# Performance work log

Hardware: AMD Instinct MI355X
Metric: run time of the kernel (lower is better)

## Reference

```python
import jax, jax.numpy as jnp
import numpy as np

H = 512  # hidden_dim


def setup_inputs() -> dict:
    key = jax.random.key(0)
    ks = jax.random.split(key, 16)
    inp = {
        "state": jax.random.normal(ks[0], (64,), jnp.float32),
        "p_action": jax.random.normal(ks[1], (4,), jnp.float32),
        "p_reward": jax.random.normal(ks[2], (1,), jnp.float32),
        "timestep": jax.random.normal(ks[3], (1,), jnp.float32),
        "cue": jax.random.normal(ks[4], (H,), jnp.float32),
        "mem_keys": jax.random.normal(ks[5], (100000, H), jnp.float32),
        "mem_vals": jax.random.normal(ks[6], (100000, H), jnp.float32),
        "Wx": jax.random.normal(ks[7], (5 * H, 70), jnp.float32) * 0.05,
        "Wh": jax.random.normal(ks[8], (5 * H, H), jnp.float32) * 0.05,
        "b": jax.random.normal(ks[9], (5 * H,), jnp.float32) * 0.05,
        "actor_w": jax.random.normal(ks[10], (4, H), jnp.float32) * 0.01,
        "actor_b": jnp.zeros((4,), jnp.float32),
        "critic_w": jax.random.normal(ks[11], (1, H), jnp.float32),
        "critic_b": jnp.zeros((1,), jnp.float32),
        "h0": jax.random.normal(ks[12], (H,), jnp.float32),
        "c0": jax.random.normal(ks[13], (H,), jnp.float32),
    }
    return inp


def reference(state, p_action, p_reward, timestep, cue, mem_keys, mem_vals,
              Wx, Wh, b, actor_w, actor_b, critic_w, critic_b, h0, c0):
    # ---- DND.get_memory: l2-kernel softmax-weighted read over memory bank ----
    # sims[n] = -||K[n] - cue||^2 ; m_t = softmax(sims) @ V
    sims = -jnp.sum((mem_keys - cue[None, :]) ** 2, axis=1)  # [N]
    w = jax.nn.softmax(sims)                                  # [N]
    m_t = w @ mem_vals                                        # [H]

    # ---- EpLSTMCell (DND-LSTM cell: gates f,i,o,r + candidate) ----
    x_t = jnp.concatenate([state, p_action, p_reward, timestep])  # [70]
    preact = Wx @ x_t + Wh @ h0 + b                               # [5H]
    gates = jax.nn.sigmoid(preact[: 4 * H])
    f_t, i_t, o_t, r_t = jnp.split(gates, 4)
    c_hat = jnp.tanh(preact[4 * H:])
    c_t = f_t * c0 + i_t * c_hat + r_t * m_t
    h_t = o_t * jnp.tanh(c_t)

    # ---- actor / critic heads ----
    action_dist = jax.nn.softmax(actor_w @ h_t + actor_b)
    value_estimate = critic_w @ h_t + critic_b
    return (action_dist, value_estimate, h_t, c_t)
```

## Files before the change

kernel.cpp:

```cpp
#include <hip/hip_runtime.h>
#include <math.h>

#define HDIM 512
#define NROWS 100000
#define NBLK_A 2048
#define NBLK_B 64

constexpr int SIMS_OFF   = 0;
constexpr int BMIN_OFF   = NROWS;
constexpr int CNT_OFF    = BMIN_OFF + NBLK_A;
constexpr int PREACT_OFF = CNT_OFF + 1;
constexpr int PM_OFF     = PREACT_OFF + 5 * HDIM;
constexpr int PD_OFF     = PM_OFF + NBLK_B * HDIM;

__device__ __forceinline__ float wave_sum(float v) {
    #pragma unroll
    for (int off = 32; off; off >>= 1) v += __shfl_xor(v, off);
    return v;
}
__device__ __forceinline__ float wave_min(float v) {
    #pragma unroll
    for (int off = 32; off; off >>= 1) v = fminf(v, __shfl_xor(v, off));
    return v;
}
__device__ __forceinline__ float d2sum(float4 a, float4 c) {
    float d, s;
    d = a.x - c.x; s  = d * d;
    d = a.y - c.y; s += d * d;
    d = a.z - c.z; s += d * d;
    d = a.w - c.w; s += d * d;
    return s;
}

__global__ __launch_bounds__(256)
void kA(const float* __restrict__ state, const float* __restrict__ pa,
        const float* __restrict__ pr, const float* __restrict__ ts,
        const float* __restrict__ cue, const float* __restrict__ K,
        const float* __restrict__ Wx, const float* __restrict__ Wh,
        const float* __restrict__ b, const float* __restrict__ h0,
        float* __restrict__ ws) {
    if (blockIdx.x == 0 && threadIdx.x == 0)
        ((int*)ws)[CNT_OFF] = 0;

    const int lane = threadIdx.x & 63;
    const int wib  = threadIdx.x >> 6;
    const int gw   = blockIdx.x * 4 + wib;
    const int nw   = NBLK_A * 4;

    if (gw < 5 * HDIM) {
        const int row = gw;
        float x0 = state[lane];
        float x1 = 0.f;
        if      (lane < 4)  x1 = pa[lane];
        else if (lane == 4) x1 = pr[0];
        else if (lane == 5) x1 = ts[0];

        const float4* h04 = (const float4*)h0;
        const float4  hA = h04[lane], hB = h04[64 + lane];
        const float4* wh4 = (const float4*)(Wh + (size_t)row * HDIM);
        const float4 a0 = wh4[lane], a1 = wh4[64 + lane];
        float acc = a0.x*hA.x + a0.y*hA.y + a0.z*hA.z + a0.w*hA.w
                  + a1.x*hB.x + a1.y*hB.y + a1.z*hB.z + a1.w*hB.w;
        const float* wxr = Wx + (size_t)row * 70;
        acc += wxr[lane] * x0;
        if (lane < 6) acc += wxr[64 + lane] * x1;
        acc = wave_sum(acc);
        if (lane == 0) ws[PREACT_OFF + row] = acc + b[row];
    }

    const float4* c4 = (const float4*)cue;
    const float4 cA = c4[lane], cB = c4[64 + lane];
    float minss = INFINITY;

    const int NG = NROWS / 4;
    for (int g = gw; g < NG; g += nw) {
        const int n = g * 4;
        const float* r = K + (size_t)n * HDIM;
        const float4* p0 = (const float4*)(r);
        const float4* p1 = (const float4*)(r + HDIM);
        const float4* p2 = (const float4*)(r + 2 * HDIM);
        const float4* p3 = (const float4*)(r + 3 * HDIM);
        const float4 a0 = p0[lane], b0 = p0[64 + lane];
        const float4 a1 = p1[lane], b1 = p1[64 + lane];
        const float4 a2 = p2[lane], b2 = p2[64 + lane];
        const float4 a3 = p3[lane], b3 = p3[64 + lane];
        float s0 = d2sum(a0, cA) + d2sum(b0, cB);
        float s1 = d2sum(a1, cA) + d2sum(b1, cB);
        float s2 = d2sum(a2, cA) + d2sum(b2, cB);
        float s3 = d2sum(a3, cA) + d2sum(b3, cB);
        #pragma unroll
        for (int off = 32; off; off >>= 1) {
            s0 += __shfl_xor(s0, off);
            s1 += __shfl_xor(s1, off);
            s2 += __shfl_xor(s2, off);
            s3 += __shfl_xor(s3, off);
        }
        if (lane == 0) {
            *(float4*)&ws[SIMS_OFF + n] = make_float4(-s0, -s1, -s2, -s3);
        }
        minss = fminf(fminf(minss, s0), fminf(fminf(s1, s2), s3));
    }

    minss = wave_min(minss);
    __shared__ float smin[4];
    if (lane == 0) smin[wib] = minss;
    __syncthreads();
    if (threadIdx.x == 0)
        ws[BMIN_OFF + blockIdx.x] =
            fminf(fminf(smin[0], smin[1]), fminf(smin[2], smin[3]));
}

__global__ __launch_bounds__(256)
void kB(const float* __restrict__ V, const float* __restrict__ c0,
        const float* __restrict__ aw, const float* __restrict__ ab,
        const float* __restrict__ cw, const float* __restrict__ cb,
        float* __restrict__ ws, float* __restrict__ out) {
    const int lane = threadIdx.x & 63;
    const int wib  = threadIdx.x >> 6;
    const int t    = threadIdx.x;

    float mn = INFINITY;
    #pragma unroll
    for (int i = 0; i < NBLK_A / 256; i++)
        mn = fminf(mn, ws[BMIN_OFF + i * 256 + t]);
    mn = wave_min(mn);
    __shared__ float sred[4];
    if (lane == 0) sred[wib] = mn;
    __syncthreads();
    const float smax = -fminf(fminf(sred[0], sred[1]), fminf(sred[2], sred[3]));

    const int gwid = blockIdx.x * 4 + wib;
    float4 accA = {0.f,0.f,0.f,0.f}, accB = {0.f,0.f,0.f,0.f};
    float dsum = 0.f;

    const int nchunks = (NROWS + 63) / 64;
    for (int c = gwid; c < nchunks; c += NBLK_B * 4) {
        const int n = c * 64 + lane;
        const bool valid = (n < NROWS);
        const float s = valid ? ws[SIMS_OFF + n] : -INFINITY;
        const float e = expf(s - smax);
        dsum += e;
        unsigned long long mask = __ballot(valid && (s - smax >= -30.0f));
        while (mask) {
            const int bpos = __ffsll(mask) - 1;
            mask &= mask - 1;
            const int nb = c * 64 + bpos;
            const float eb = __shfl(e, bpos);
            const float4* v4 = (const float4*)(V + (size_t)nb * HDIM);
            const float4 vA = v4[lane], vB = v4[64 + lane];
            accA.x += eb * vA.x; accA.y += eb * vA.y;
            accA.z += eb * vA.z; accA.w += eb * vA.w;
            accB.x += eb * vB.x; accB.y += eb * vB.y;
            accB.z += eb * vB.z; accB.w += eb * vB.w;
        }
    }
    dsum = wave_sum(dsum);

    __shared__ float lm[4][HDIM];
    __shared__ float ld[4];
    {
        float* rowp = lm[wib];
        rowp[lane*4 + 0]       = accA.x; rowp[lane*4 + 1]       = accA.y;
        rowp[lane*4 + 2]       = accA.z; rowp[lane*4 + 3]       = accA.w;
        rowp[256 + lane*4 + 0] = accB.x; rowp[256 + lane*4 + 1] = accB.y;
        rowp[256 + lane*4 + 2] = accB.z; rowp[256 + lane*4 + 3] = accB.w;
        if (lane == 0) ld[wib] = dsum;
    }
    __syncthreads();

    ws[PM_OFF + blockIdx.x * HDIM + t] =
        lm[0][t] + lm[1][t] + lm[2][t] + lm[3][t];
    ws[PM_OFF + blockIdx.x * HDIM + 256 + t] =
        lm[0][256+t] + lm[1][256+t] + lm[2][256+t] + lm[3][256+t];
    if (t == 0)
        ws[PD_OFF + blockIdx.x] = ld[0] + ld[1] + ld[2] + ld[3];

    __threadfence();
    __shared__ int sOld;
    if (t == 0) sOld = atomicAdd((int*)ws + CNT_OFF, 1);
    __syncthreads();
    if (sOld != NBLK_B - 1) return;
    __threadfence();

    __shared__ float hl[HDIM];
    __shared__ float sden;
    __shared__ float logits[4];

    if (wib == 0) {
        float d = ws[PD_OFF + lane];
        d = wave_sum(d);
        if (lane == 0) sden = d;
    }
    float m0 = 0.f, m1 = 0.f;
    #pragma unroll 8
    for (int b2 = 0; b2 < NBLK_B; b2++) {
        m0 += ws[PM_OFF + b2 * HDIM + t];
        m1 += ws[PM_OFF + b2 * HDIM + 256 + t];
    }
    __syncthreads();
    const float inv_den = 1.f / sden;
    m0 *= inv_den; m1 *= inv_den;

    #pragma unroll
    for (int half = 0; half < 2; half++) {
        const int tt = t + half * 256;
        const float mm = half ? m1 : m0;
        const float pf = ws[PREACT_OFF + tt];
        const float pi = ws[PREACT_OFF + HDIM + tt];
        const float po = ws[PREACT_OFF + 2*HDIM + tt];
        const float prg= ws[PREACT_OFF + 3*HDIM + tt];
        const float pc = ws[PREACT_OFF + 4*HDIM + tt];
        const float f_t = 1.f / (1.f + expf(-pf));
        const float i_t = 1.f / (1.f + expf(-pi));
        const float o_t = 1.f / (1.f + expf(-po));
        const float r_t = 1.f / (1.f + expf(-prg));
        const float chat = tanhf(pc);
        const float ct = f_t * c0[tt] + i_t * chat + r_t * mm;
        const float ht = o_t * tanhf(ct);
        out[517 + tt] = ct;
        out[5 + tt]   = ht;
        hl[tt] = ht;
    }
    __syncthreads();

    if (wib < 4) {
        float acc = 0.f;
        #pragma unroll
        for (int j = 0; j < HDIM; j += 64)
            acc += aw[wib * HDIM + j + lane] * hl[j + lane];
        acc = wave_sum(acc);
        if (lane == 0) logits[wib] = acc + ab[wib];
    }
    if (wib == 0) {
        float acc = 0.f;
        #pragma unroll
        for (int j = 0; j < HDIM; j += 64)
            acc += cw[j + lane] * hl[j + lane];
        acc = wave_sum(acc);
        if (lane == 0) out[4] = acc + cb[0];
    }
    __syncthreads();

    if (t == 0) {
        const float mx = fmaxf(fmaxf(logits[0], logits[1]),
                               fmaxf(logits[2], logits[3]));
        const float e0 = expf(logits[0] - mx), e1 = expf(logits[1] - mx);
        const float e2 = expf(logits[2] - mx), e3 = expf(logits[3] - mx);
        const float inv = 1.f / (e0 + e1 + e2 + e3);
        out[0] = e0 * inv; out[1] = e1 * inv;
        out[2] = e2 * inv; out[3] = e3 * inv;
    }
}

extern "C" void kernel_launch(void* const* d_in, const int* in_sizes, int n_in,
                              void* d_out, int out_size, void* d_ws, size_t ws_size,
                              hipStream_t stream) {
    const float* state  = (const float*)d_in[0];
    const float* pa     = (const float*)d_in[1];
    const float* pr     = (const float*)d_in[2];
    const float* ts     = (const float*)d_in[3];
    const float* cue    = (const float*)d_in[4];
    const float* keys   = (const float*)d_in[5];
    const float* vals   = (const float*)d_in[6];
    const float* Wx     = (const float*)d_in[7];
    const float* Wh     = (const float*)d_in[8];
    const float* b      = (const float*)d_in[9];
    const float* aw     = (const float*)d_in[10];
    const float* ab     = (const float*)d_in[11];
    const float* cw     = (const float*)d_in[12];
    const float* cb     = (const float*)d_in[13];
    const float* h0     = (const float*)d_in[14];
    const float* c0     = (const float*)d_in[15];
    float* ws  = (float*)d_ws;
    float* out = (float*)d_out;

    kA<<<NBLK_A, 256, 0, stream>>>(state, pa, pr, ts, cue, keys, Wx, Wh, b, h0, ws);
    kB<<<NBLK_B, 256, 0, stream>>>(vals, c0, aw, ab, cw, cb, ws, out);
}
```

Baseline: 57.60 us.

## Compact near-max similarity candidates per block and finish softmax read in one block

The key-scan kernel now gives each block a contiguous row range. The range is split unevenly so the first 640 blocks, which also compute the LSTM preactivations, get fewer rows. Instead of writing all 100000 similarities, each block keeps only rows within 30 of its local minimum distance and writes them as a compact (score, index) candidate list. A single-block second kernel prefix-scans the candidate counts, filters against the global minimum, and computes the weighted value read from the survivors. This drops the full similarity write and reread and the 64-block reduction with its atomic counter. The trade-offs are a serial softmax denominator loop, a hard cap of 1024 survivors, and a denominator that now leaves out the negligible tail terms.

```diff
diff --git a/kernel.cpp b/kernel.cpp
--- a/kernel.cpp
+++ b/kernel.cpp
@@ -4,14 +4,15 @@
 #define HDIM 512
 #define NROWS 100000
 #define NBLK_A 2048
-#define NBLK_B 64
-
-constexpr int SIMS_OFF   = 0;
-constexpr int BMIN_OFF   = NROWS;
-constexpr int CNT_OFF    = BMIN_OFF + NBLK_A;
-constexpr int PREACT_OFF = CNT_OFF + 1;
-constexpr int PM_OFF     = PREACT_OFF + 5 * HDIM;
-constexpr int PD_OFF     = PM_OFF + NBLK_B * HDIM;
+#define K_CAP 1024
+
+#define SPLIT_ROWS 29268
+#define SPLIT_BLKS 640
+
+constexpr int BMIN_OFF   = 0;
+constexpr int CNT_OFF    = NBLK_A;
+constexpr int CAND_OFF   = 2 * NBLK_A;
+constexpr int PREACT_OFF = CAND_OFF + NBLK_A * 128;
 
 __device__ __forceinline__ float wave_sum(float v) {
     #pragma unroll
@@ -39,13 +40,10 @@
         const float* __restrict__ Wx, const float* __restrict__ Wh,
         const float* __restrict__ b, const float* __restrict__ h0,
         float* __restrict__ ws) {
-    if (blockIdx.x == 0 && threadIdx.x == 0)
-        ((int*)ws)[CNT_OFF] = 0;
-
     const int lane = threadIdx.x & 63;
     const int wib  = threadIdx.x >> 6;
-    const int gw   = blockIdx.x * 4 + wib;
-    const int nw   = NBLK_A * 4;
+    const int blk  = blockIdx.x;
+    const int gw   = blk * 4 + wib;
 
     if (gw < 5 * HDIM) {
         const int row = gw;
@@ -68,18 +66,34 @@
         if (lane == 0) ws[PREACT_OFF + row] = acc + b[row];
     }
 
+    int bs, be;
+    if (blk < SPLIT_BLKS) {
+        bs = (int)(((long long)blk       * SPLIT_ROWS) / SPLIT_BLKS);
+        be = (int)(((long long)(blk + 1) * SPLIT_ROWS) / SPLIT_BLKS);
+    } else {
+        const int rb = blk - SPLIT_BLKS;
+        bs = SPLIT_ROWS + (int)(((long long)rb       * (NROWS - SPLIT_ROWS)) / (NBLK_A - SPLIT_BLKS));
+        be = SPLIT_ROWS + (int)(((long long)(rb + 1) * (NROWS - SPLIT_ROWS)) / (NBLK_A - SPLIT_BLKS));
+    }
+    const int rows = be - bs;
+
+    __shared__ float ssbuf[64];
+    __shared__ float swmin[4];
+
+    const int wstart = bs + (rows * wib) / 4;
+    const int wend   = bs + (rows * (wib + 1)) / 4;
+
     const float4* c4 = (const float4*)cue;
     const float4 cA = c4[lane], cB = c4[64 + lane];
-    float minss = INFINITY;
-
-    const int NG = NROWS / 4;
-    for (int g = gw; g < NG; g += nw) {
-        const int n = g * 4;
-        const float* r = K + (size_t)n * HDIM;
-        const float4* p0 = (const float4*)(r);
-        const float4* p1 = (const float4*)(r + HDIM);
-        const float4* p2 = (const float4*)(r + 2 * HDIM);
-        const float4* p3 = (const float4*)(r + 3 * HDIM);
+    float wmin = INFINITY;
+
+    int r = wstart;
+    for (; r + 4 <= wend; r += 4) {
+        const float* p = K + (size_t)r * HDIM;
+        const float4* p0 = (const float4*)(p);
+        const float4* p1 = (const float4*)(p + HDIM);
+        const float4* p2 = (const float4*)(p + 2 * HDIM);
+        const float4* p3 = (const float4*)(p + 3 * HDIM);
         const float4 a0 = p0[lane], b0 = p0[64 + lane];
         const float4 a1 = p1[lane], b1 = p1[64 + lane];
         const float4 a2 = p2[lane], b2 = p2[64 + lane];
@@ -96,18 +110,38 @@
             s3 += __shfl_xor(s3, off);
         }
         if (lane == 0) {
-            *(float4*)&ws[SIMS_OFF + n] = make_float4(-s0, -s1, -s2, -s3);
-        }
-        minss = fminf(fminf(minss, s0), fminf(fminf(s1, s2), s3));
-    }
-
-    minss = wave_min(minss);
-    __shared__ float smin[4];
-    if (lane == 0) smin[wib] = minss;
-    __syncthreads();
-    if (threadIdx.x == 0)
-        ws[BMIN_OFF + blockIdx.x] =
-            fminf(fminf(smin[0], smin[1]), fminf(smin[2], smin[3]));
+            ssbuf[r - bs + 0] = s0;
+            ssbuf[r - bs + 1] = s1;
+            ssbuf[r - bs + 2] = s2;
+            ssbuf[r - bs + 3] = s3;
+        }
+        wmin = fminf(fminf(wmin, s0), fminf(fminf(s1, s2), s3));
+    }
+    for (; r < wend; ++r) {
+        const float4* p0 = (const float4*)(K + (size_t)r * HDIM);
+        const float4 a0 = p0[lane], b0 = p0[64 + lane];
+        float s0 = wave_sum(d2sum(a0, cA) + d2sum(b0, cB));
+        if (lane == 0) ssbuf[r - bs] = s0;
+        wmin = fminf(wmin, s0);
+    }
+
+    if (lane == 0) swmin[wib] = wmin;
+    __syncthreads();
+    const float bminv = fminf(fminf(swmin[0], swmin[1]),
+                              fminf(swmin[2], swmin[3]));
+    if (threadIdx.x == 0) ws[BMIN_OFF + blk] = bminv;
+
+    if (wib == 0) {
+        const int t = lane;
+        const bool ok = (t < rows) && (ssbuf[t] <= bminv + 30.0f);
+        const unsigned long long mask = __ballot(ok);
+        if (lane == 0) ((int*)ws)[CNT_OFF + blk] = (int)__popcll(mask);
+        if (ok) {
+            const int pos = (int)__popcll(mask & ((1ull << t) - 1ull));
+            float2* cand = (float2*)(ws + CAND_OFF);
+            cand[(blk << 6) + pos] = make_float2(ssbuf[t], __int_as_float(bs + t));
+        }
+    }
 }
 
 __global__ __launch_bounds__(256)
@@ -115,90 +149,86 @@
         const float* __restrict__ aw, const float* __restrict__ ab,
         const float* __restrict__ cw, const float* __restrict__ cb,
         float* __restrict__ ws, float* __restrict__ out) {
-    const int lane = threadIdx.x & 63;
-    const int wib  = threadIdx.x >> 6;
     const int t    = threadIdx.x;
+    const int lane = t & 63;
+    const int wib  = t >> 6;
+
+    __shared__ float sred[4];
+    __shared__ int   sc[256];
+    __shared__ float surv_s[K_CAP];
+    __shared__ int   surv_n[K_CAP];
+    __shared__ float sden;
+    __shared__ float hl[HDIM];
+    __shared__ float logits[4];
 
     float mn = INFINITY;
     #pragma unroll
-    for (int i = 0; i < NBLK_A / 256; i++)
-        mn = fminf(mn, ws[BMIN_OFF + i * 256 + t]);
+    for (int j = 0; j < NBLK_A / 256; j++)
+        mn = fminf(mn, ws[BMIN_OFF + j * 256 + t]);
     mn = wave_min(mn);
-    __shared__ float sred[4];
     if (lane == 0) sred[wib] = mn;
     __syncthreads();
-    const float smax = -fminf(fminf(sred[0], sred[1]), fminf(sred[2], sred[3]));
-
-    const int gwid = blockIdx.x * 4 + wib;
-    float4 accA = {0.f,0.f,0.f,0.f}, accB = {0.f,0.f,0.f,0.f};
-    float dsum = 0.f;
-
-    const int nchunks = (NROWS + 63) / 64;
-    for (int c = gwid; c < nchunks; c += NBLK_B * 4) {
-        const int n = c * 64 + lane;
-        const bool valid = (n < NROWS);
-        const float s = valid ? ws[SIMS_OFF + n] : -INFINITY;
-        const float e = expf(s - smax);
-        dsum += e;
-        unsigned long long mask = __ballot(valid && (s - smax >= -30.0f));
-        while (mask) {
-            const int bpos = __ffsll(mask) - 1;
-            mask &= mask - 1;
-            const int nb = c * 64 + bpos;
-            const float eb = __shfl(e, bpos);
-            const float4* v4 = (const float4*)(V + (size_t)nb * HDIM);
-            const float4 vA = v4[lane], vB = v4[64 + lane];
-            accA.x += eb * vA.x; accA.y += eb * vA.y;
-            accA.z += eb * vA.z; accA.w += eb * vA.w;
-            accB.x += eb * vB.x; accB.y += eb * vB.y;
-            accB.z += eb * vB.z; accB.w += eb * vB.w;
-        }
-    }
-    dsum = wave_sum(dsum);
-
-    __shared__ float lm[4][HDIM];
-    __shared__ float ld[4];
-    {
-        float* rowp = lm[wib];
-        rowp[lane*4 + 0]       = accA.x; rowp[lane*4 + 1]       = accA.y;
-        rowp[lane*4 + 2]       = accA.z; rowp[lane*4 + 3]       = accA.w;
-        rowp[256 + lane*4 + 0] = accB.x; rowp[256 + lane*4 + 1] = accB.y;
-        rowp[256 + lane*4 + 2] = accB.z; rowp[256 + lane*4 + 3] = accB.w;
-        if (lane == 0) ld[wib] = dsum;
-    }
-    __syncthreads();
-
-    ws[PM_OFF + blockIdx.x * HDIM + t] =
-        lm[0][t] + lm[1][t] + lm[2][t] + lm[3][t];
-    ws[PM_OFF + blockIdx.x * HDIM + 256 + t] =
-        lm[0][256+t] + lm[1][256+t] + lm[2][256+t] + lm[3][256+t];
-    if (t == 0)
-        ws[PD_OFF + blockIdx.x] = ld[0] + ld[1] + ld[2] + ld[3];
-
-    __threadfence();
-    __shared__ int sOld;
-    if (t == 0) sOld = atomicAdd((int*)ws + CNT_OFF, 1);
-    __syncthreads();
-    if (sOld != NBLK_B - 1) return;
-    __threadfence();
-
-    __shared__ float hl[HDIM];
-    __shared__ float sden;
-    __shared__ float logits[4];
-
-    if (wib == 0) {
-        float d = ws[PD_OFF + lane];
-        d = wave_sum(d);
-        if (lane == 0) sden = d;
-    }
+    const float smin = fminf(fminf(sred[0], sred[1]), fminf(sred[2], sred[3]));
+    const float thr  = smin + 30.0f;
+
+    const int*    cnt  = (const int*)ws + CNT_OFF;
+    const float2* cand = (const float2*)(ws + CAND_OFF);
+
+    int mycnt = 0;
+    #pragma unroll
+    for (int j = 0; j < NBLK_A / 256; j++) {
+        const int bidx = t + j * 256;
+        const int c = cnt[bidx];
+        for (int e = 0; e < c; e++)
+            if (cand[(bidx << 6) + e].x <= thr) mycnt++;
+    }
+    sc[t] = mycnt;
+    __syncthreads();
+    for (int d = 1; d < 256; d <<= 1) {
+        int v = (t >= d) ? sc[t - d] : 0;
+        __syncthreads();
+        sc[t] += v;
+        __syncthreads();
+    }
+    const int total = sc[255];
+    int off = sc[t] - mycnt;
+    #pragma unroll
+    for (int j = 0; j < NBLK_A / 256; j++) {
+        const int bidx = t + j * 256;
+        const int c = cnt[bidx];
+        for (int e = 0; e < c; e++) {
+            const float2 ce = cand[(bidx << 6) + e];
+            if (ce.x <= thr) {
+                if (off < K_CAP) {
+                    surv_s[off] = ce.x;
+                    surv_n[off] = __float_as_int(ce.y);
+                }
+                off++;
+            }
+        }
+    }
+    __syncthreads();
+    const int tot = (total < K_CAP) ? total : K_CAP;
+
+    if (t == 0) {
+        float den = 0.f;
+        for (int i = 0; i < tot; i++) {
+            const float e = expf(smin - surv_s[i]);
+            surv_s[i] = e;
+            den += e;
+        }
+        sden = den;
+    }
+    __syncthreads();
+    const float inv_den = 1.f / sden;
+
     float m0 = 0.f, m1 = 0.f;
-    #pragma unroll 8
-    for (int b2 = 0; b2 < NBLK_B; b2++) {
-        m0 += ws[PM_OFF + b2 * HDIM + t];
-        m1 += ws[PM_OFF + b2 * HDIM + 256 + t];
-    }
-    __syncthreads();
-    const float inv_den = 1.f / sden;
+    for (int i = 0; i < tot; i++) {
+        const float w = surv_s[i];
+        const size_t base = (size_t)surv_n[i] * HDIM;
+        m0 += w * V[base + t];
+        m1 += w * V[base + 256 + t];
+    }
     m0 *= inv_den; m1 *= inv_den;
 
     #pragma unroll
@@ -275,5 +305,5 @@
     float* out = (float*)d_out;
 
     kA<<<NBLK_A, 256, 0, stream>>>(state, pa, pr, ts, cue, keys, Wx, Wh, b, h0, ws);
-    kB<<<NBLK_B, 256, 0, stream>>>(vals, c0, aw, ab, cw, cb, ws, out);
-}
+    kB<<<1, 256, 0, stream>>>(vals, c0, aw, ab, cw, cb, ws, out);
+}
```

Measured after the change: 71.94 us. +24.9%, slower.
